# Kernel tuning notes

Measured on AMD Instinct MI355X. Metric: run time of the kernel, lower is better.

Reference implementation:

```python
import jax, jax.numpy as jnp
import numpy as np

EPS = 1e-5
NUM_GROUPS = 32
HT_MIN = -2.0
HT_MAX = 2.0


def setup_inputs() -> dict:
    key = jax.random.key(0)
    k1, k2 = jax.random.split(key)
    B, Cin, Cout, H, W = 32, 256, 512, 56, 56
    x = jax.random.normal(k1, (B, Cin, H, W), dtype=jnp.float32)
    weight = jax.random.normal(k2, (Cout, Cin), dtype=jnp.float32)
    gamma = jnp.ones((Cout,), dtype=jnp.float32)
    beta = jnp.zeros((Cout,), dtype=jnp.float32)
    return {"x": x, "weight": weight, "gamma": gamma, "beta": beta}


def reference(x, weight, gamma, beta) -> jnp.ndarray:
    B, Cin, H, W = x.shape
    Cout = weight.shape[0]
    G = NUM_GROUPS
    # 1x1-conv style GEMM over channels (no bias in the original kernel call)
    y = jnp.einsum("oc,bchw->bohw", weight, x)  # [B, Cout, H, W]
    # GroupNorm: stats over (channels-in-group, H, W) per sample
    yg = y.reshape(B, G, Cout // G, H, W)
    mean = jnp.mean(yg, axis=(2, 3, 4), keepdims=True)
    var = jnp.var(yg, axis=(2, 3, 4), keepdims=True)
    yn = ((yg - mean) * jax.lax.rsqrt(var + EPS)).reshape(B, Cout, H, W)
    yn = yn * gamma[None, :, None, None] + beta[None, :, None, None]
    # HardTanh clamp
    return jnp.clip(yn, HT_MIN, HT_MAX)
```

## Files before the change

### kernel.cpp

```cpp
#include <hip/hip_runtime.h>


#define HW    3136
#define CIN   256
#define COUT  512
#define BATCH 32
#define NG    32
#define CPG   16
#define EPS   1e-5f

typedef _Float16 f16x8 __attribute__((ext_vector_type(8)));
typedef float    f32x4 __attribute__((ext_vector_type(4)));
typedef unsigned int u32;

__device__ __forceinline__ void gload16(const void* g, void* l) {
  __builtin_amdgcn_global_load_lds(
      (const u32 __attribute__((address_space(1)))*)g,
      (u32 __attribute__((address_space(3)))*)l, 16, 0, 0);
}

__global__ __launch_bounds__(256) void k0_transpose(
    const float* __restrict__ x, const float* __restrict__ w,
    _Float16* __restrict__ xT, _Float16* __restrict__ wf,
    float* __restrict__ stats)
{
  __shared__ float T[64 * 65];
  const int bid = blockIdx.x;
  const int t   = threadIdx.x;
  const int b   = bid / 196;
  const int r   = bid % 196;
  const int st  = r >> 2;
  const int ct  = r & 3;
  const int s0  = st * 64, c0 = ct * 64;

  const float* xb = x + ((size_t)b * CIN + c0) * HW + s0;
#pragma unroll
  for (int rr = 0; rr < 4; ++rr) {
    const int c_loc = (t >> 4) + rr * 16;
    const int s4    = (t & 15) * 4;
    const float4 v  = *(const float4*)(xb + (size_t)c_loc * HW + s4);
    T[(s4 + 0) * 65 + c_loc] = v.x;
    T[(s4 + 1) * 65 + c_loc] = v.y;
    T[(s4 + 2) * 65 + c_loc] = v.z;
    T[(s4 + 3) * 65 + c_loc] = v.w;
  }
  __syncthreads();
#pragma unroll
  for (int p = 0; p < 2; ++p) {
    const int s_loc = p * 32 + (t >> 3);
    const int cg    = (t & 7) * 8;
    f16x8 o;
#pragma unroll
    for (int j = 0; j < 8; ++j) o[j] = (_Float16)T[s_loc * 65 + cg + j];
    *(f16x8*)(xT + ((size_t)b * HW + s0 + s_loc) * CIN + c0 + cg) = o;
  }
  if (bid < (COUT * CIN) / 256) wf[bid * 256 + t] = (_Float16)w[bid * 256 + t];
  if (bid < 8)                  stats[bid * 256 + t] = 0.f;
}

template<int WRITE_OUT>
__global__ __launch_bounds__(256) void k_gemm(
    const _Float16* __restrict__ xT, const _Float16* __restrict__ wf,
    float* __restrict__ stats, const float* __restrict__ mr,
    const float* __restrict__ gamma, const float* __restrict__ beta,
    float* __restrict__ out)
{
  __shared__ __align__(16) _Float16 As[128 * 64];
  __shared__ __align__(16) _Float16 Bs[128 * 64];

  const int bid  = blockIdx.x;
  const int tile = (bid & 7) * 400 + (bid >> 3);
  const int mt   = tile & 3;
  const int q2   = tile >> 2;
  const int nt   = q2 % 25;
  const int b    = q2 / 25;
  const int s0   = (nt == 24) ? (HW - 128) : nt * 128;

  const int t    = threadIdx.x;
  const int lane = t & 63;
  const int wid  = t >> 6;
  const int wy   = wid >> 1, wx = wid & 1;
  const int lr   = lane >> 3;
  const int ccg  = (lane & 7) ^ lr;

  f32x4 acc[4][4] = {};
  const _Float16* xb = xT + (size_t)b * HW * CIN;

  for (int kt = 0; kt < 4; ++kt) {
    __syncthreads();
    const int ko = kt * 64;
#pragma unroll
    for (int u = 0; u < 4; ++u) {
      const int rowb = (wid * 4 + u) * 8 + lr;
      gload16(wf + (size_t)(mt * 128 + rowb) * CIN + ko + ccg * 8,
              As + (wid * 4 + u) * 512);
      gload16(xb + (size_t)(s0 + rowb) * CIN + ko + ccg * 8,
              Bs + (wid * 4 + u) * 512);
    }
    __syncthreads();
#pragma unroll
    for (int ks = 0; ks < 2; ++ks) {
      const int c = ks * 4 + (lane >> 4);
      f16x8 af[4], bfr[4];
#pragma unroll
      for (int mi = 0; mi < 4; ++mi) {
        const int m = wy * 64 + mi * 16 + (lane & 15);
        af[mi] = *(const f16x8*)(As + m * 64 + ((c ^ (m & 7)) * 8));
      }
#pragma unroll
      for (int ni = 0; ni < 4; ++ni) {
        const int n = wx * 64 + ni * 16 + (lane & 15);
        bfr[ni] = *(const f16x8*)(Bs + n * 64 + ((c ^ (n & 7)) * 8));
      }
#pragma unroll
      for (int mi = 0; mi < 4; ++mi)
#pragma unroll
        for (int ni = 0; ni < 4; ++ni)
          acc[mi][ni] = __builtin_amdgcn_mfma_f32_16x16x32_f16(
              af[mi], bfr[ni], acc[mi][ni], 0, 0, 0);
    }
  }

  if (WRITE_OUT == 0) {
    const int slo  = (nt == 24) ? 3072 : 0;
    const int colb = s0 + wx * 64 + (lane & 15);
#pragma unroll
    for (int mi = 0; mi < 4; ++mi) {
      float s1 = 0.f, s2 = 0.f;
#pragma unroll
      for (int ni = 0; ni < 4; ++ni) {
        if (colb + ni * 16 >= slo) {
#pragma unroll
          for (int rr = 0; rr < 4; ++rr) {
            const float v = acc[mi][ni][rr];
            s1 += v; s2 += v * v;
          }
        }
      }
#pragma unroll
      for (int off = 32; off > 0; off >>= 1) {
        s1 += __shfl_down(s1, off, 64);
        s2 += __shfl_down(s2, off, 64);
      }
      if (lane == 0) {
        const int g = mt * 8 + wy * 4 + mi;
        atomicAdd(&stats[(b * NG + g) * 2 + 0], s1);
        atomicAdd(&stats[(b * NG + g) * 2 + 1], s2);
      }
    }
  } else {
#pragma unroll
    for (int mi = 0; mi < 4; ++mi) {
      const int g = mt * 8 + wy * 4 + mi;
      const float mean = mr[(b * NG + g) * 2 + 0];
      const float rsig = mr[(b * NG + g) * 2 + 1];
      const int row0 = mt * 128 + wy * 64 + mi * 16 + ((lane >> 4) << 2);
#pragma unroll
      for (int rr = 0; rr < 4; ++rr) {
        const int co = row0 + rr;
        const float sc = rsig * gamma[co];
        const float sh = beta[co] - mean * sc;
        float* orow = out + ((size_t)b * COUT + co) * HW + s0 + wx * 64 + (lane & 15);
#pragma unroll
        for (int ni = 0; ni < 4; ++ni) {
          float v = acc[mi][ni][rr] * sc + sh;
          v = fminf(fmaxf(v, -2.0f), 2.0f);
          orow[ni * 16] = v;
        }
      }
    }
  }
}

__global__ void k_finalize(const float* __restrict__ stats, float* __restrict__ mr)
{
  const int i = blockIdx.x * 256 + threadIdx.x;
  if (i < BATCH * NG) {
    const float cnt  = (float)(CPG * HW);
    const float mean = stats[i * 2] / cnt;
    const float var  = stats[i * 2 + 1] / cnt - mean * mean;
    mr[i * 2]     = mean;
    mr[i * 2 + 1] = rsqrtf(var + EPS);
  }
}

extern "C" void kernel_launch(void* const* d_in, const int* in_sizes, int n_in,
                              void* d_out, int out_size, void* d_ws, size_t ws_size,
                              hipStream_t stream)
{
  const float* x     = (const float*)d_in[0];
  const float* w     = (const float*)d_in[1];
  const float* gamma = (const float*)d_in[2];
  const float* beta  = (const float*)d_in[3];
  float* out = (float*)d_out;

  const size_t xT_bytes = (size_t)BATCH * HW * CIN * 2;
  const size_t wf_bytes = (size_t)COUT * CIN * 2;
  char* ws = (char*)d_ws;
  _Float16* xT = (_Float16*)ws;
  _Float16* wf = (_Float16*)(ws + xT_bytes);
  float* stats = (float*)(ws + xT_bytes + wf_bytes);
  float* mr    = (float*)(ws + xT_bytes + wf_bytes + 8192);

  if (ws_size < xT_bytes + wf_bytes + 16384) return;

  k0_transpose<<<dim3(BATCH * 196), dim3(256), 0, stream>>>(x, w, xT, wf, stats);
  k_gemm<0><<<dim3(BATCH * 100), dim3(256), 0, stream>>>(
      xT, wf, stats, nullptr, nullptr, nullptr, nullptr);
  k_finalize<<<dim3(4), dim3(256), 0, stream>>>(stats, mr);
  k_gemm<1><<<dim3(BATCH * 100), dim3(256), 0, stream>>>(
      xT, wf, nullptr, mr, gamma, beta, out);
}
```

Measured before the change: 402.3 us.

## Materialize fp16 GEMM output once instead of recomputing GEMM for normalization

```diff
diff --git a/kernel.cpp b/kernel.cpp
--- a/kernel.cpp
+++ b/kernel.cpp
@@ -58,12 +58,9 @@
   if (bid < 8)                  stats[bid * 256 + t] = 0.f;
 }
 
-template<int WRITE_OUT>
 __global__ __launch_bounds__(256) void k_gemm(
     const _Float16* __restrict__ xT, const _Float16* __restrict__ wf,
-    float* __restrict__ stats, const float* __restrict__ mr,
-    const float* __restrict__ gamma, const float* __restrict__ beta,
-    float* __restrict__ out)
+    float* __restrict__ stats, _Float16* __restrict__ y)
 {
   __shared__ __align__(16) _Float16 As[128 * 64];
   __shared__ __align__(16) _Float16 Bs[128 * 64];
@@ -121,67 +118,85 @@
     }
   }
 
-  if (WRITE_OUT == 0) {
-    const int slo  = (nt == 24) ? 3072 : 0;
-    const int colb = s0 + wx * 64 + (lane & 15);
-#pragma unroll
-    for (int mi = 0; mi < 4; ++mi) {
-      float s1 = 0.f, s2 = 0.f;
-#pragma unroll
-      for (int ni = 0; ni < 4; ++ni) {
-        if (colb + ni * 16 >= slo) {
-#pragma unroll
-          for (int rr = 0; rr < 4; ++rr) {
-            const float v = acc[mi][ni][rr];
-            s1 += v; s2 += v * v;
-          }
+  const int slo  = (nt == 24) ? 3072 : 0;
+  const int colb = s0 + wx * 64 + (lane & 15);
+#pragma unroll
+  for (int mi = 0; mi < 4; ++mi) {
+    float s1 = 0.f, s2 = 0.f;
+#pragma unroll
+    for (int ni = 0; ni < 4; ++ni) {
+      if (colb + ni * 16 >= slo) {
+#pragma unroll
+        for (int rr = 0; rr < 4; ++rr) {
+          const float v = acc[mi][ni][rr];
+          s1 += v; s2 += v * v;
         }
       }
-#pragma unroll
-      for (int off = 32; off > 0; off >>= 1) {
-        s1 += __shfl_down(s1, off, 64);
-        s2 += __shfl_down(s2, off, 64);
-      }
-      if (lane == 0) {
-        const int g = mt * 8 + wy * 4 + mi;
-        atomicAdd(&stats[(b * NG + g) * 2 + 0], s1);
-        atomicAdd(&stats[(b * NG + g) * 2 + 1], s2);
-      }
-    }
-  } else {
-#pragma unroll
-    for (int mi = 0; mi < 4; ++mi) {
+    }
+#pragma unroll
+    for (int off = 32; off > 0; off >>= 1) {
+      s1 += __shfl_down(s1, off, 64);
+      s2 += __shfl_down(s2, off, 64);
+    }
+    if (lane == 0) {
       const int g = mt * 8 + wy * 4 + mi;
-      const float mean = mr[(b * NG + g) * 2 + 0];
-      const float rsig = mr[(b * NG + g) * 2 + 1];
-      const int row0 = mt * 128 + wy * 64 + mi * 16 + ((lane >> 4) << 2);
-#pragma unroll
-      for (int rr = 0; rr < 4; ++rr) {
-        const int co = row0 + rr;
-        const float sc = rsig * gamma[co];
-        const float sh = beta[co] - mean * sc;
-        float* orow = out + ((size_t)b * COUT + co) * HW + s0 + wx * 64 + (lane & 15);
-#pragma unroll
-        for (int ni = 0; ni < 4; ++ni) {
-          float v = acc[mi][ni][rr] * sc + sh;
-          v = fminf(fmaxf(v, -2.0f), 2.0f);
-          orow[ni * 16] = v;
-        }
-      }
-    }
-  }
-}
-
-__global__ void k_finalize(const float* __restrict__ stats, float* __restrict__ mr)
+      atomicAdd(&stats[(b * NG + g) * 2 + 0], s1);
+      atomicAdd(&stats[(b * NG + g) * 2 + 1], s2);
+    }
+    const int row0 = mt * 128 + wy * 64 + mi * 16 + ((lane >> 4) << 2);
+#pragma unroll
+    for (int rr = 0; rr < 4; ++rr) {
+      _Float16* yrow = y + ((size_t)b * COUT + row0 + rr) * HW + colb;
+#pragma unroll
+      for (int ni = 0; ni < 4; ++ni)
+        yrow[ni * 16] = (_Float16)acc[mi][ni][rr];
+    }
+  }
+}
+
+__global__ __launch_bounds__(256) void k_finalize(
+    const float* __restrict__ stats, const float* __restrict__ gamma,
+    const float* __restrict__ beta, float* __restrict__ ss)
 {
   const int i = blockIdx.x * 256 + threadIdx.x;
-  if (i < BATCH * NG) {
+  if (i < BATCH * COUT) {
+    const int b  = i >> 9;
+    const int co = i & (COUT - 1);
+    const int g  = co >> 4;
     const float cnt  = (float)(CPG * HW);
-    const float mean = stats[i * 2] / cnt;
-    const float var  = stats[i * 2 + 1] / cnt - mean * mean;
-    mr[i * 2]     = mean;
-    mr[i * 2 + 1] = rsqrtf(var + EPS);
-  }
+    const float s1   = stats[(b * NG + g) * 2 + 0];
+    const float s2   = stats[(b * NG + g) * 2 + 1];
+    const float mean = s1 / cnt;
+    const float var  = s2 / cnt - mean * mean;
+    const float rsig = rsqrtf(var + EPS);
+    const float sc   = rsig * gamma[co];
+    ss[i * 2 + 0] = sc;
+    ss[i * 2 + 1] = beta[co] - mean * sc;
+  }
+}
+
+__global__ __launch_bounds__(256) void k_norm(
+    const _Float16* __restrict__ y, const float* __restrict__ ss,
+    float* __restrict__ out)
+{
+  const u32 u   = blockIdx.x * 256 + threadIdx.x;
+  const u32 row = u / (HW / 8);
+  const u32 sp  = (u - row * (HW / 8)) * 8;
+  const float sc = ss[row * 2 + 0];
+  const float sh = ss[row * 2 + 1];
+  const f16x8 v = *(const f16x8*)(y + (size_t)row * HW + sp);
+  float4 o0, o1;
+  o0.x = fminf(fmaxf((float)v[0] * sc + sh, -2.0f), 2.0f);
+  o0.y = fminf(fmaxf((float)v[1] * sc + sh, -2.0f), 2.0f);
+  o0.z = fminf(fmaxf((float)v[2] * sc + sh, -2.0f), 2.0f);
+  o0.w = fminf(fmaxf((float)v[3] * sc + sh, -2.0f), 2.0f);
+  o1.x = fminf(fmaxf((float)v[4] * sc + sh, -2.0f), 2.0f);
+  o1.y = fminf(fmaxf((float)v[5] * sc + sh, -2.0f), 2.0f);
+  o1.z = fminf(fmaxf((float)v[6] * sc + sh, -2.0f), 2.0f);
+  o1.w = fminf(fmaxf((float)v[7] * sc + sh, -2.0f), 2.0f);
+  float* op = out + (size_t)row * HW + sp;
+  *(float4*)(op)     = o0;
+  *(float4*)(op + 4) = o1;
 }
 
 extern "C" void kernel_launch(void* const* d_in, const int* in_sizes, int n_in,
@@ -196,18 +211,21 @@
 
   const size_t xT_bytes = (size_t)BATCH * HW * CIN * 2;
   const size_t wf_bytes = (size_t)COUT * CIN * 2;
+  const size_t st_bytes = 8192;
+  const size_t ss_bytes = (size_t)BATCH * COUT * 2 * 4;
+  const size_t y_bytes  = (size_t)BATCH * COUT * HW * 2;
+
   char* ws = (char*)d_ws;
   _Float16* xT = (_Float16*)ws;
   _Float16* wf = (_Float16*)(ws + xT_bytes);
   float* stats = (float*)(ws + xT_bytes + wf_bytes);
-  float* mr    = (float*)(ws + xT_bytes + wf_bytes + 8192);
-
-  if (ws_size < xT_bytes + wf_bytes + 16384) return;
+  float* ss    = (float*)(ws + xT_bytes + wf_bytes + st_bytes);
+  _Float16* y  = (_Float16*)(ws + xT_bytes + wf_bytes + st_bytes + ss_bytes);
+
+  if (ws_size < xT_bytes + wf_bytes + st_bytes + ss_bytes + y_bytes) return;
 
   k0_transpose<<<dim3(BATCH * 196), dim3(256), 0, stream>>>(x, w, xT, wf, stats);
-  k_gemm<0><<<dim3(BATCH * 100), dim3(256), 0, stream>>>(
-      xT, wf, stats, nullptr, nullptr, nullptr, nullptr);
-  k_finalize<<<dim3(4), dim3(256), 0, stream>>>(stats, mr);
-  k_gemm<1><<<dim3(BATCH * 100), dim3(256), 0, stream>>>(
-      xT, wf, nullptr, mr, gamma, beta, out);
-}
+  k_gemm<<<dim3(BATCH * 100), dim3(256), 0, stream>>>(xT, wf, stats, y);
+  k_finalize<<<dim3(BATCH * COUT / 256), dim3(256), 0, stream>>>(stats, gamma, beta, ss);
+  k_norm<<<dim3(BATCH * COUT * HW / 8 / 256), dim3(256), 0, stream>>>(y, ss, out);
+}
```

New measurement: 401.4 us. Within noise of the previous version (-0.2%).
